# Kernel tuning notes

Hardware: AMD Instinct MI355X
Metric: run time of the kernel (lower is better)

Reference implementation:

```python
import jax, jax.numpy as jnp
import numpy as np

HIDDEN = 512
NUM_HEAD = 8
HEAD_DIM = HIDDEN // NUM_HEAD


def setup_inputs() -> dict:
    key = jax.random.key(0)
    ks = jax.random.split(key, 12)
    B, S = 8, 1024
    inp = {
        "v": jax.random.normal(ks[0], (B, S, HIDDEN), dtype=jnp.float32),
        "k": jax.random.normal(ks[1], (B, S, HIDDEN), dtype=jnp.float32),
        "q": jax.random.normal(ks[2], (B, S, HIDDEN), dtype=jnp.float32),
        "mask": jnp.zeros((B, 1, 1, S), dtype=bool),
    }
    scale = 1.0 / np.sqrt(HIDDEN)
    inp["Wv"] = jax.random.normal(ks[3], (HIDDEN, HIDDEN), dtype=jnp.float32) * scale
    inp["bv"] = jax.random.normal(ks[4], (HIDDEN,), dtype=jnp.float32) * scale
    inp["Wk"] = jax.random.normal(ks[5], (HIDDEN, HIDDEN), dtype=jnp.float32) * scale
    inp["bk"] = jax.random.normal(ks[6], (HIDDEN,), dtype=jnp.float32) * scale
    inp["Wq"] = jax.random.normal(ks[7], (HIDDEN, HIDDEN), dtype=jnp.float32) * scale
    inp["bq"] = jax.random.normal(ks[8], (HIDDEN,), dtype=jnp.float32) * scale
    inp["Wm"] = jax.random.normal(ks[9], (HIDDEN, HIDDEN), dtype=jnp.float32) * scale
    inp["bm"] = jax.random.normal(ks[10], (HIDDEN,), dtype=jnp.float32) * scale
    return inp


def _split_heads(x):
    # [B, S, H*D] -> [B, H, S, D]
    B, S, _ = x.shape
    return x.reshape(B, S, NUM_HEAD, HEAD_DIM).transpose(0, 2, 1, 3)


def reference(v, k, q, mask, Wv, bv, Wk, bk, Wq, bq, Wm, bm):
    B, S, _ = q.shape
    # linear projections (torch Linear: x @ W.T + b)
    vh = _split_heads(v @ Wv.T + bv)
    kh = _split_heads(k @ Wk.T + bk)
    qh = _split_heads(q @ Wq.T + bq)
    scale = 1.0 / jnp.sqrt(jnp.asarray(HEAD_DIM, dtype=qh.dtype))
    scores = jnp.einsum('bhqd,bhkd->bhqk', qh, kh) * scale
    scores = jnp.where(mask, jnp.asarray(-10000.0, dtype=scores.dtype), scores)
    att_map = jax.nn.softmax(scores, axis=-1)
    atted = jnp.einsum('bhqk,bhkd->bhqd', att_map, vh)
    atted = atted.transpose(0, 2, 1, 3).reshape(B, S, HIDDEN)
    atted = atted @ Wm.T + bm
    return atted, att_map
```

## Files before the change

### kernel.cpp

```cpp
#include <hip/hip_runtime.h>
#include <cstddef>

#define SEQ 1024
#define HID 512
#define NH 8
#define HD 64

typedef __attribute__((ext_vector_type(8))) short bf16x8;
typedef __attribute__((ext_vector_type(4))) float f32x4;

__device__ inline unsigned short f2bf(float f) {
  unsigned u = __builtin_bit_cast(unsigned, f);
  return (unsigned short)((u + 0x7fffu + ((u >> 16) & 1u)) >> 16);
}

template <int MODE>
__global__ __launch_bounds__(256) void proj_mfma(const void* __restrict__ Xv,
                                                 const float* __restrict__ W,
                                                 const float* __restrict__ bias,
                                                 void* __restrict__ outv) {
  __shared__ short As[128 * 64];
  __shared__ short Bs[128 * 64];

  const int t = threadIdx.x;
  const int lane = t & 63, wid = t >> 6;
  const int lg = lane >> 4, lr = lane & 15;
  const int wm = (wid >> 1) * 64, wn = (wid & 1) * 64;
  const int m0 = blockIdx.y * 128, n0 = blockIdx.x * 128;

  f32x4 acc[4][4];
  const f32x4 zf = {0.f, 0.f, 0.f, 0.f};
#pragma unroll
  for (int mg = 0; mg < 4; ++mg)
#pragma unroll
    for (int ng = 0; ng < 4; ++ng) acc[mg][ng] = zf;

  for (int k0 = 0; k0 < 512; k0 += 64) {
    __syncthreads();
#pragma unroll
    for (int i = 0; i < 4; ++i) {
      const int gi = t + i * 256;
      const int r = gi >> 3, g = gi & 7;
      const int dst = r * 64 + ((g ^ (r & 7)) * 8);
      if (MODE == 2) {
        const unsigned short* Xb = (const unsigned short*)Xv;
        *reinterpret_cast<bf16x8*>(As + dst) =
            *reinterpret_cast<const bf16x8*>(Xb + (size_t)(m0 + r) * 512 + k0 + g * 8);
      } else {
        const float* X = (const float*)Xv;
        const float* src = X + (size_t)(m0 + r) * 512 + k0 + g * 8;
        const float4 a = *reinterpret_cast<const float4*>(src);
        const float4 b2 = *reinterpret_cast<const float4*>(src + 4);
        union { bf16x8 v; unsigned short u[8]; } p;
        p.u[0] = f2bf(a.x);  p.u[1] = f2bf(a.y);  p.u[2] = f2bf(a.z);  p.u[3] = f2bf(a.w);
        p.u[4] = f2bf(b2.x); p.u[5] = f2bf(b2.y); p.u[6] = f2bf(b2.z); p.u[7] = f2bf(b2.w);
        *reinterpret_cast<bf16x8*>(As + dst) = p.v;
      }
      const float* srcw = W + (size_t)(n0 + r) * 512 + k0 + g * 8;
      const float4 wa = *reinterpret_cast<const float4*>(srcw);
      const float4 wb = *reinterpret_cast<const float4*>(srcw + 4);
      union { bf16x8 v; unsigned short u[8]; } q;
      q.u[0] = f2bf(wa.x); q.u[1] = f2bf(wa.y); q.u[2] = f2bf(wa.z); q.u[3] = f2bf(wa.w);
      q.u[4] = f2bf(wb.x); q.u[5] = f2bf(wb.y); q.u[6] = f2bf(wb.z); q.u[7] = f2bf(wb.w);
      *reinterpret_cast<bf16x8*>(Bs + dst) = q.v;
    }
    __syncthreads();

#pragma unroll
    for (int c = 0; c < 2; ++c) {
      bf16x8 af[4], bf[4];
#pragma unroll
      for (int mg = 0; mg < 4; ++mg) {
        const int r = wm + mg * 16 + lr;
        af[mg] = *reinterpret_cast<const bf16x8*>(As + r * 64 + (((lg + 4 * c) ^ (r & 7)) * 8));
      }
#pragma unroll
      for (int ng = 0; ng < 4; ++ng) {
        const int r = wn + ng * 16 + lr;
        bf[ng] = *reinterpret_cast<const bf16x8*>(Bs + r * 64 + (((lg + 4 * c) ^ (r & 7)) * 8));
      }
#pragma unroll
      for (int mg = 0; mg < 4; ++mg)
#pragma unroll
        for (int ng = 0; ng < 4; ++ng)
          acc[mg][ng] =
              __builtin_amdgcn_mfma_f32_16x16x32_bf16(af[mg], bf[ng], acc[mg][ng], 0, 0, 0);
    }
  }

  float bv[4];
#pragma unroll
  for (int ng = 0; ng < 4; ++ng) bv[ng] = bias[n0 + wn + ng * 16 + lr];

#pragma unroll
  for (int mg = 0; mg < 4; ++mg) {
#pragma unroll
    for (int reg = 0; reg < 4; ++reg) {
      const int m = m0 + wm + mg * 16 + 4 * lg + reg;
#pragma unroll
      for (int ng = 0; ng < 4; ++ng) {
        const int n = n0 + wn + ng * 16 + lr;
        float cval = acc[mg][ng][reg] + bv[ng];
        if (MODE == 2) {
          ((float*)outv)[(size_t)m * 512 + n] = cval;
        } else {
          if (MODE == 1) cval *= 0.125f;
          const int b = m >> 10, s = m & 1023, h = n >> 6, d = n & 63;
          ((unsigned short*)outv)[(((size_t)(b * NH + h)) * SEQ + s) * HD + d] = f2bf(cval);
        }
      }
    }
  }
}

__global__ __launch_bounds__(256) void attn_mfma(const unsigned short* __restrict__ qh,
                                                 const unsigned short* __restrict__ kh,
                                                 const unsigned short* __restrict__ vh,
                                                 const unsigned char* __restrict__ mask,
                                                 float* __restrict__ att_map,
                                                 unsigned short* __restrict__ atted) {
  __shared__ short Ks[128 * 64];
  __shared__ short Vt[64 * 128];
  __shared__ short Ps[4][2048];

  const int t = threadIdx.x;
  const int lane = t & 63, wid = t >> 6;
  const int lg = lane >> 4, lr = lane & 15;
  const int qt = blockIdx.x & 15;
  const int bh = blockIdx.x >> 4;
  const int b = bh >> 3, h = bh & 7;
  const int q0 = qt * 64 + wid * 16;

  const unsigned short* Qb = qh + ((size_t)bh * SEQ + q0) * HD;
  const unsigned short* Kb = kh + (size_t)bh * SEQ * HD;
  const unsigned short* Vb = vh + (size_t)bh * SEQ * HD;
  const unsigned char* mrow = mask + (size_t)b * SEQ;

  bf16x8 qf[2];
#pragma unroll
  for (int c = 0; c < 2; ++c)
    qf[c] = *reinterpret_cast<const bf16x8*>(Qb + (size_t)lr * HD + lg * 8 + 32 * c);

  float rs0 = 0.f, rs1 = 0.f, rs2 = 0.f, rs3 = 0.f;
  for (int kt = 0; kt < 8; ++kt) {
    __syncthreads();
#pragma unroll
    for (int i = 0; i < 4; ++i) {
      const int gi = t + i * 256;
      const int r = gi >> 3, g = gi & 7;
      *reinterpret_cast<bf16x8*>(Ks + r * 64 + ((g ^ (r & 7)) * 8)) =
          *reinterpret_cast<const bf16x8*>(Kb + (size_t)(kt * 128 + r) * HD + g * 8);
    }
    __syncthreads();
#pragma unroll
    for (int cg = 0; cg < 8; ++cg) {
      f32x4 s = {0.f, 0.f, 0.f, 0.f};
#pragma unroll
      for (int c = 0; c < 2; ++c) {
        const int r = cg * 16 + lr;
        const bf16x8 kf =
            *reinterpret_cast<const bf16x8*>(Ks + r * 64 + (((lg + 4 * c) ^ (r & 7)) * 8));
        s = __builtin_amdgcn_mfma_f32_16x16x32_bf16(qf[c], kf, s, 0, 0, 0);
      }
      const int kpos = kt * 128 + cg * 16 + lr;
      if (!mrow[kpos]) {
        rs0 += __expf(s[0]); rs1 += __expf(s[1]);
        rs2 += __expf(s[2]); rs3 += __expf(s[3]);
      }
    }
  }
#pragma unroll
  for (int m = 1; m <= 8; m <<= 1) {
    rs0 += __shfl_xor(rs0, m); rs1 += __shfl_xor(rs1, m);
    rs2 += __shfl_xor(rs2, m); rs3 += __shfl_xor(rs3, m);
  }
  const float inv0 = 1.f / rs0, inv1 = 1.f / rs1, inv2 = 1.f / rs2, inv3 = 1.f / rs3;

  const f32x4 zf = {0.f, 0.f, 0.f, 0.f};
  f32x4 oacc[4] = {zf, zf, zf, zf};
  short* Pw = Ps[wid];

  for (int kt = 0; kt < 8; ++kt) {
    __syncthreads();
#pragma unroll
    for (int i = 0; i < 4; ++i) {
      const int gi = t + i * 256;
      const int r = gi >> 3, g = gi & 7;
      *reinterpret_cast<bf16x8*>(Ks + r * 64 + ((g ^ (r & 7)) * 8)) =
          *reinterpret_cast<const bf16x8*>(Kb + (size_t)(kt * 128 + r) * HD + g * 8);
      union { bf16x8 v; unsigned short u[8]; } vv;
      vv.v = *reinterpret_cast<const bf16x8*>(Vb + (size_t)(kt * 128 + r) * HD + g * 8);
#pragma unroll
      for (int j = 0; j < 8; ++j) {
        const int d = g * 8 + j;
        Vt[d * 128 + (((r >> 3) ^ (d & 7)) * 8) + (r & 7)] = (short)vv.u[j];
      }
    }
    __syncthreads();

#pragma unroll
    for (int cg = 0; cg < 8; ++cg) {
      f32x4 s = {0.f, 0.f, 0.f, 0.f};
#pragma unroll
      for (int c = 0; c < 2; ++c) {
        const int r = cg * 16 + lr;
        const bf16x8 kf =
            *reinterpret_cast<const bf16x8*>(Ks + r * 64 + (((lg + 4 * c) ^ (r & 7)) * 8));
        s = __builtin_amdgcn_mfma_f32_16x16x32_bf16(qf[c], kf, s, 0, 0, 0);
      }
      const int kpos = kt * 128 + cg * 16 + lr;
      const bool msk = mrow[kpos];
      float p[4];
      p[0] = msk ? 0.f : __expf(s[0]) * inv0;
      p[1] = msk ? 0.f : __expf(s[1]) * inv1;
      p[2] = msk ? 0.f : __expf(s[2]) * inv2;
      p[3] = msk ? 0.f : __expf(s[3]) * inv3;
      const int col = cg * 16 + lr;
#pragma unroll
      for (int reg = 0; reg < 4; ++reg) {
        const int row = 4 * lg + reg;
        att_map[((size_t)bh * SEQ + (q0 + row)) * SEQ + kpos] = p[reg];
        Pw[row * 128 + (((col >> 3) ^ (row & 7)) * 8) + (col & 7)] = (short)f2bf(p[reg]);
      }
    }

    bf16x8 pa[4];
#pragma unroll
    for (int c = 0; c < 4; ++c)
      pa[c] = *reinterpret_cast<const bf16x8*>(Pw + lr * 128 + (((lg + 4 * c) ^ (lr & 7)) * 8));
#pragma unroll
    for (int ng = 0; ng < 4; ++ng) {
      const int d = ng * 16 + lr;
#pragma unroll
      for (int c = 0; c < 4; ++c) {
        const bf16x8 vf =
            *reinterpret_cast<const bf16x8*>(Vt + d * 128 + (((lg + 4 * c) ^ (d & 7)) * 8));
        oacc[ng] = __builtin_amdgcn_mfma_f32_16x16x32_bf16(pa[c], vf, oacc[ng], 0, 0, 0);
      }
    }
  }

#pragma unroll
  for (int ng = 0; ng < 4; ++ng) {
#pragma unroll
    for (int reg = 0; reg < 4; ++reg) {
      const int q = q0 + 4 * lg + reg;
      const int d = ng * 16 + lr;
      atted[((size_t)b * SEQ + q) * HID + h * HD + d] = f2bf(oacc[ng][reg]);
    }
  }
}

extern "C" void kernel_launch(void* const* d_in, const int* in_sizes, int n_in,
                              void* d_out, int out_size, void* d_ws, size_t ws_size,
                              hipStream_t stream) {
  const float* v = (const float*)d_in[0];
  const float* k = (const float*)d_in[1];
  const float* q = (const float*)d_in[2];
  const unsigned char* mask = (const unsigned char*)d_in[3];
  const float* Wv = (const float*)d_in[4];
  const float* bv = (const float*)d_in[5];
  const float* Wk = (const float*)d_in[6];
  const float* bk = (const float*)d_in[7];
  const float* Wq = (const float*)d_in[8];
  const float* bq = (const float*)d_in[9];
  const float* Wm = (const float*)d_in[10];
  const float* bm = (const float*)d_in[11];

  float* out_atted = (float*)d_out;
  float* out_att = out_atted + (size_t)8 * SEQ * HID;

  const size_t TN = (size_t)8 * SEQ * HID;
  unsigned short* qh = (unsigned short*)d_ws;
  unsigned short* kh = qh + TN;
  unsigned short* vh = kh + TN;
  unsigned short* aw = vh + TN;

  const dim3 gg(4, 64);
  proj_mfma<1><<<gg, 256, 0, stream>>>(q, Wq, bq, qh);
  proj_mfma<0><<<gg, 256, 0, stream>>>(k, Wk, bk, kh);
  proj_mfma<0><<<gg, 256, 0, stream>>>(v, Wv, bv, vh);

  attn_mfma<<<dim3(1024), 256, 0, stream>>>(qh, kh, vh, mask, out_att, aw);

  proj_mfma<2><<<gg, 256, 0, stream>>>(aw, Wm, bm, out_atted);
}
```

Measured before the change: 228.5 us.

## Single-pass attention with register-held probabilities and merged QKV projection launch

Removes the separate row-sum pass over K by accumulating exp scores and the unnormalized P·V in one sweep. Unnormalized bf16 probabilities are kept in registers, normalized once at the end, and written to att_map as vectorized nontemporal stores; the output rows are scaled by the inverse sum. The mask becomes an additive float table in shared memory, and the three QKV projections are merged into one launch via blockIdx.z. In exchange, att_map is now derived from bf16-rounded probabilities, which loses precision, and the 64-entry register array raises VGPR pressure.

```diff
diff --git a/kernel.cpp b/kernel.cpp
--- a/kernel.cpp
+++ b/kernel.cpp
@@ -13,14 +13,28 @@
   unsigned u = __builtin_bit_cast(unsigned, f);
   return (unsigned short)((u + 0x7fffu + ((u >> 16) & 1u)) >> 16);
 }
-
-template <int MODE>
-__global__ __launch_bounds__(256) void proj_mfma(const void* __restrict__ Xv,
-                                                 const float* __restrict__ W,
-                                                 const float* __restrict__ bias,
-                                                 void* __restrict__ outv) {
+__device__ inline float bfhi2f(unsigned u) {
+  return __builtin_bit_cast(float, u & 0xffff0000u);
+}
+__device__ inline float bflo2f(unsigned u) {
+  return __builtin_bit_cast(float, u << 16);
+}
+
+__global__ __launch_bounds__(256) void proj_qkv(
+    const float* __restrict__ x0, const float* __restrict__ x1, const float* __restrict__ x2,
+    const float* __restrict__ w0, const float* __restrict__ w1, const float* __restrict__ w2,
+    const float* __restrict__ b0, const float* __restrict__ b1, const float* __restrict__ b2,
+    unsigned short* __restrict__ o0, unsigned short* __restrict__ o1,
+    unsigned short* __restrict__ o2) {
   __shared__ short As[128 * 64];
   __shared__ short Bs[128 * 64];
+
+  const int z = blockIdx.z;
+  const float* X = z == 0 ? x0 : (z == 1 ? x1 : x2);
+  const float* W = z == 0 ? w0 : (z == 1 ? w1 : w2);
+  const float* bias = z == 0 ? b0 : (z == 1 ? b1 : b2);
+  unsigned short* out = z == 0 ? o0 : (z == 1 ? o1 : o2);
+  const float scale = z == 0 ? 0.125f : 1.0f;
 
   const int t = threadIdx.x;
   const int lane = t & 63, wid = t >> 6;
@@ -42,12 +56,7 @@
       const int gi = t + i * 256;
       const int r = gi >> 3, g = gi & 7;
       const int dst = r * 64 + ((g ^ (r & 7)) * 8);
-      if (MODE == 2) {
-        const unsigned short* Xb = (const unsigned short*)Xv;
-        *reinterpret_cast<bf16x8*>(As + dst) =
-            *reinterpret_cast<const bf16x8*>(Xb + (size_t)(m0 + r) * 512 + k0 + g * 8);
-      } else {
-        const float* X = (const float*)Xv;
+      {
         const float* src = X + (size_t)(m0 + r) * 512 + k0 + g * 8;
         const float4 a = *reinterpret_cast<const float4*>(src);
         const float4 b2 = *reinterpret_cast<const float4*>(src + 4);
@@ -56,6 +65,89 @@
         p.u[4] = f2bf(b2.x); p.u[5] = f2bf(b2.y); p.u[6] = f2bf(b2.z); p.u[7] = f2bf(b2.w);
         *reinterpret_cast<bf16x8*>(As + dst) = p.v;
       }
+      {
+        const float* srcw = W + (size_t)(n0 + r) * 512 + k0 + g * 8;
+        const float4 wa = *reinterpret_cast<const float4*>(srcw);
+        const float4 wb = *reinterpret_cast<const float4*>(srcw + 4);
+        union { bf16x8 v; unsigned short u[8]; } q;
+        q.u[0] = f2bf(wa.x); q.u[1] = f2bf(wa.y); q.u[2] = f2bf(wa.z); q.u[3] = f2bf(wa.w);
+        q.u[4] = f2bf(wb.x); q.u[5] = f2bf(wb.y); q.u[6] = f2bf(wb.z); q.u[7] = f2bf(wb.w);
+        *reinterpret_cast<bf16x8*>(Bs + dst) = q.v;
+      }
+    }
+    __syncthreads();
+
+#pragma unroll
+    for (int c = 0; c < 2; ++c) {
+      bf16x8 af[4], bfr[4];
+#pragma unroll
+      for (int mg = 0; mg < 4; ++mg) {
+        const int r = wm + mg * 16 + lr;
+        af[mg] = *reinterpret_cast<const bf16x8*>(As + r * 64 + (((lg + 4 * c) ^ (r & 7)) * 8));
+      }
+#pragma unroll
+      for (int ng = 0; ng < 4; ++ng) {
+        const int r = wn + ng * 16 + lr;
+        bfr[ng] = *reinterpret_cast<const bf16x8*>(Bs + r * 64 + (((lg + 4 * c) ^ (r & 7)) * 8));
+      }
+#pragma unroll
+      for (int mg = 0; mg < 4; ++mg)
+#pragma unroll
+        for (int ng = 0; ng < 4; ++ng)
+          acc[mg][ng] =
+              __builtin_amdgcn_mfma_f32_16x16x32_bf16(af[mg], bfr[ng], acc[mg][ng], 0, 0, 0);
+    }
+  }
+
+  float bv[4];
+#pragma unroll
+  for (int ng = 0; ng < 4; ++ng) bv[ng] = bias[n0 + wn + ng * 16 + lr];
+
+#pragma unroll
+  for (int mg = 0; mg < 4; ++mg) {
+#pragma unroll
+    for (int reg = 0; reg < 4; ++reg) {
+      const int m = m0 + wm + mg * 16 + 4 * lg + reg;
+#pragma unroll
+      for (int ng = 0; ng < 4; ++ng) {
+        const int n = n0 + wn + ng * 16 + lr;
+        const float cval = (acc[mg][ng][reg] + bv[ng]) * scale;
+        const int b = m >> 10, s = m & 1023, h = n >> 6, d = n & 63;
+        out[(((size_t)(b * NH + h)) * SEQ + s) * HD + d] = f2bf(cval);
+      }
+    }
+  }
+}
+
+__global__ __launch_bounds__(256) void proj_out(const unsigned short* __restrict__ Xb,
+                                                const float* __restrict__ W,
+                                                const float* __restrict__ bias,
+                                                float* __restrict__ outv) {
+  __shared__ short As[128 * 64];
+  __shared__ short Bs[128 * 64];
+
+  const int t = threadIdx.x;
+  const int lane = t & 63, wid = t >> 6;
+  const int lg = lane >> 4, lr = lane & 15;
+  const int wm = (wid >> 1) * 64, wn = (wid & 1) * 64;
+  const int m0 = blockIdx.y * 128, n0 = blockIdx.x * 128;
+
+  f32x4 acc[4][4];
+  const f32x4 zf = {0.f, 0.f, 0.f, 0.f};
+#pragma unroll
+  for (int mg = 0; mg < 4; ++mg)
+#pragma unroll
+    for (int ng = 0; ng < 4; ++ng) acc[mg][ng] = zf;
+
+  for (int k0 = 0; k0 < 512; k0 += 64) {
+    __syncthreads();
+#pragma unroll
+    for (int i = 0; i < 4; ++i) {
+      const int gi = t + i * 256;
+      const int r = gi >> 3, g = gi & 7;
+      const int dst = r * 64 + ((g ^ (r & 7)) * 8);
+      *reinterpret_cast<bf16x8*>(As + dst) =
+          *reinterpret_cast<const bf16x8*>(Xb + (size_t)(m0 + r) * 512 + k0 + g * 8);
       const float* srcw = W + (size_t)(n0 + r) * 512 + k0 + g * 8;
       const float4 wa = *reinterpret_cast<const float4*>(srcw);
       const float4 wb = *reinterpret_cast<const float4*>(srcw + 4);
@@ -68,7 +160,7 @@
 
 #pragma unroll
     for (int c = 0; c < 2; ++c) {
-      bf16x8 af[4], bf[4];
+      bf16x8 af[4], bfr[4];
 #pragma unroll
       for (int mg = 0; mg < 4; ++mg) {
         const int r = wm + mg * 16 + lr;
@@ -77,14 +169,14 @@
 #pragma unroll
       for (int ng = 0; ng < 4; ++ng) {
         const int r = wn + ng * 16 + lr;
-        bf[ng] = *reinterpret_cast<const bf16x8*>(Bs + r * 64 + (((lg + 4 * c) ^ (r & 7)) * 8));
+        bfr[ng] = *reinterpret_cast<const bf16x8*>(Bs + r * 64 + (((lg + 4 * c) ^ (r & 7)) * 8));
       }
 #pragma unroll
       for (int mg = 0; mg < 4; ++mg)
 #pragma unroll
         for (int ng = 0; ng < 4; ++ng)
           acc[mg][ng] =
-              __builtin_amdgcn_mfma_f32_16x16x32_bf16(af[mg], bf[ng], acc[mg][ng], 0, 0, 0);
+              __builtin_amdgcn_mfma_f32_16x16x32_bf16(af[mg], bfr[ng], acc[mg][ng], 0, 0, 0);
     }
   }
 
@@ -100,14 +192,7 @@
 #pragma unroll
       for (int ng = 0; ng < 4; ++ng) {
         const int n = n0 + wn + ng * 16 + lr;
-        float cval = acc[mg][ng][reg] + bv[ng];
-        if (MODE == 2) {
-          ((float*)outv)[(size_t)m * 512 + n] = cval;
-        } else {
-          if (MODE == 1) cval *= 0.125f;
-          const int b = m >> 10, s = m & 1023, h = n >> 6, d = n & 63;
-          ((unsigned short*)outv)[(((size_t)(b * NH + h)) * SEQ + s) * HD + d] = f2bf(cval);
-        }
+        __builtin_nontemporal_store(acc[mg][ng][reg] + bv[ng], outv + (size_t)m * 512 + n);
       }
     }
   }
@@ -121,7 +206,8 @@
                                                  unsigned short* __restrict__ atted) {
   __shared__ short Ks[128 * 64];
   __shared__ short Vt[64 * 128];
-  __shared__ short Ps[4][2048];
+  __shared__ short Pw4[4][2048];
+  __shared__ float maskf[1024];
 
   const int t = threadIdx.x;
   const int lane = t & 63, wid = t >> 6;
@@ -136,50 +222,24 @@
   const unsigned short* Vb = vh + (size_t)bh * SEQ * HD;
   const unsigned char* mrow = mask + (size_t)b * SEQ;
 
+#pragma unroll
+  for (int i = 0; i < 4; ++i) {
+    const int idx = t + i * 256;
+    maskf[idx] = mrow[idx] ? -10000.f : 0.f;
+  }
+
   bf16x8 qf[2];
 #pragma unroll
   for (int c = 0; c < 2; ++c)
     qf[c] = *reinterpret_cast<const bf16x8*>(Qb + (size_t)lr * HD + lg * 8 + 32 * c);
 
-  float rs0 = 0.f, rs1 = 0.f, rs2 = 0.f, rs3 = 0.f;
-  for (int kt = 0; kt < 8; ++kt) {
-    __syncthreads();
-#pragma unroll
-    for (int i = 0; i < 4; ++i) {
-      const int gi = t + i * 256;
-      const int r = gi >> 3, g = gi & 7;
-      *reinterpret_cast<bf16x8*>(Ks + r * 64 + ((g ^ (r & 7)) * 8)) =
-          *reinterpret_cast<const bf16x8*>(Kb + (size_t)(kt * 128 + r) * HD + g * 8);
-    }
-    __syncthreads();
-#pragma unroll
-    for (int cg = 0; cg < 8; ++cg) {
-      f32x4 s = {0.f, 0.f, 0.f, 0.f};
-#pragma unroll
-      for (int c = 0; c < 2; ++c) {
-        const int r = cg * 16 + lr;
-        const bf16x8 kf =
-            *reinterpret_cast<const bf16x8*>(Ks + r * 64 + (((lg + 4 * c) ^ (r & 7)) * 8));
-        s = __builtin_amdgcn_mfma_f32_16x16x32_bf16(qf[c], kf, s, 0, 0, 0);
-      }
-      const int kpos = kt * 128 + cg * 16 + lr;
-      if (!mrow[kpos]) {
-        rs0 += __expf(s[0]); rs1 += __expf(s[1]);
-        rs2 += __expf(s[2]); rs3 += __expf(s[3]);
-      }
-    }
-  }
-#pragma unroll
-  for (int m = 1; m <= 8; m <<= 1) {
-    rs0 += __shfl_xor(rs0, m); rs1 += __shfl_xor(rs1, m);
-    rs2 += __shfl_xor(rs2, m); rs3 += __shfl_xor(rs3, m);
-  }
-  const float inv0 = 1.f / rs0, inv1 = 1.f / rs1, inv2 = 1.f / rs2, inv3 = 1.f / rs3;
-
+  uint2 pk[64];
+  float rs = 0.f;
   const f32x4 zf = {0.f, 0.f, 0.f, 0.f};
   f32x4 oacc[4] = {zf, zf, zf, zf};
-  short* Pw = Ps[wid];
-
+  short* Pw = Pw4[wid];
+
+#pragma unroll
   for (int kt = 0; kt < 8; ++kt) {
     __syncthreads();
 #pragma unroll
@@ -200,53 +260,69 @@
 
 #pragma unroll
     for (int cg = 0; cg < 8; ++cg) {
-      f32x4 s = {0.f, 0.f, 0.f, 0.f};
+      f32x4 s = zf;
 #pragma unroll
       for (int c = 0; c < 2; ++c) {
         const int r = cg * 16 + lr;
         const bf16x8 kf =
             *reinterpret_cast<const bf16x8*>(Ks + r * 64 + (((lg + 4 * c) ^ (r & 7)) * 8));
-        s = __builtin_amdgcn_mfma_f32_16x16x32_bf16(qf[c], kf, s, 0, 0, 0);
-      }
-      const int kpos = kt * 128 + cg * 16 + lr;
-      const bool msk = mrow[kpos];
-      float p[4];
-      p[0] = msk ? 0.f : __expf(s[0]) * inv0;
-      p[1] = msk ? 0.f : __expf(s[1]) * inv1;
-      p[2] = msk ? 0.f : __expf(s[2]) * inv2;
-      p[3] = msk ? 0.f : __expf(s[3]) * inv3;
-      const int col = cg * 16 + lr;
-#pragma unroll
-      for (int reg = 0; reg < 4; ++reg) {
-        const int row = 4 * lg + reg;
-        att_map[((size_t)bh * SEQ + (q0 + row)) * SEQ + kpos] = p[reg];
-        Pw[row * 128 + (((col >> 3) ^ (row & 7)) * 8) + (col & 7)] = (short)f2bf(p[reg]);
-      }
-    }
-
-    bf16x8 pa[4];
-#pragma unroll
-    for (int c = 0; c < 4; ++c)
-      pa[c] = *reinterpret_cast<const bf16x8*>(Pw + lr * 128 + (((lg + 4 * c) ^ (lr & 7)) * 8));
-#pragma unroll
-    for (int ng = 0; ng < 4; ++ng) {
-      const int d = ng * 16 + lr;
-#pragma unroll
-      for (int c = 0; c < 4; ++c) {
+        s = __builtin_amdgcn_mfma_f32_16x16x32_bf16(kf, qf[c], s, 0, 0, 0);
+      }
+      const float4 madd =
+          *reinterpret_cast<const float4*>(maskf + kt * 128 + cg * 16 + 4 * lg);
+      const float p0 = __expf(s[0] + madd.x);
+      const float p1 = __expf(s[1] + madd.y);
+      const float p2 = __expf(s[2] + madd.z);
+      const float p3 = __expf(s[3] + madd.w);
+      rs += (p0 + p1) + (p2 + p3);
+      uint2 pr;
+      pr.x = (unsigned)f2bf(p0) | ((unsigned)f2bf(p1) << 16);
+      pr.y = (unsigned)f2bf(p2) | ((unsigned)f2bf(p3) << 16);
+      pk[kt * 8 + cg] = pr;
+      const int gk = 2 * cg + (lg >> 1);
+      *reinterpret_cast<uint2*>(Pw + lr * 128 + ((gk ^ (lr & 7)) * 8) + (lg & 1) * 4) = pr;
+    }
+
+#pragma unroll
+    for (int c = 0; c < 4; ++c) {
+      const bf16x8 pa =
+          *reinterpret_cast<const bf16x8*>(Pw + lr * 128 + (((lg + 4 * c) ^ (lr & 7)) * 8));
+#pragma unroll
+      for (int ng = 0; ng < 4; ++ng) {
+        const int d = ng * 16 + lr;
         const bf16x8 vf =
             *reinterpret_cast<const bf16x8*>(Vt + d * 128 + (((lg + 4 * c) ^ (d & 7)) * 8));
-        oacc[ng] = __builtin_amdgcn_mfma_f32_16x16x32_bf16(pa[c], vf, oacc[ng], 0, 0, 0);
-      }
-    }
-  }
-
+        oacc[ng] = __builtin_amdgcn_mfma_f32_16x16x32_bf16(pa, vf, oacc[ng], 0, 0, 0);
+      }
+    }
+  }
+
+  rs += __shfl_xor(rs, 16);
+  rs += __shfl_xor(rs, 32);
+  const float inv = 1.f / rs;
+
+  float* arow = att_map + ((size_t)bh * SEQ + q0 + lr) * SEQ + 4 * lg;
+#pragma unroll
+  for (int cg = 0; cg < 64; ++cg) {
+    const uint2 pr = pk[cg];
+    f32x4 w;
+    w.x = bflo2f(pr.x) * inv;
+    w.y = bfhi2f(pr.x) * inv;
+    w.z = bflo2f(pr.y) * inv;
+    w.w = bfhi2f(pr.y) * inv;
+    __builtin_nontemporal_store(w, reinterpret_cast<f32x4*>(arow + cg * 16));
+  }
+
+  float invq[4];
+#pragma unroll
+  for (int reg = 0; reg < 4; ++reg) invq[reg] = __shfl(inv, 4 * lg + reg);
 #pragma unroll
   for (int ng = 0; ng < 4; ++ng) {
 #pragma unroll
     for (int reg = 0; reg < 4; ++reg) {
       const int q = q0 + 4 * lg + reg;
       const int d = ng * 16 + lr;
-      atted[((size_t)b * SEQ + q) * HID + h * HD + d] = f2bf(oacc[ng][reg]);
+      atted[((size_t)b * SEQ + q) * HID + h * HD + d] = f2bf(oacc[ng][reg] * invq[reg]);
     }
   }
 }
@@ -276,12 +352,9 @@
   unsigned short* vh = kh + TN;
   unsigned short* aw = vh + TN;
 
-  const dim3 gg(4, 64);
-  proj_mfma<1><<<gg, 256, 0, stream>>>(q, Wq, bq, qh);
-  proj_mfma<0><<<gg, 256, 0, stream>>>(k, Wk, bk, kh);
-  proj_mfma<0><<<gg, 256, 0, stream>>>(v, Wv, bv, vh);
+  proj_qkv<<<dim3(4, 64, 3), 256, 0, stream>>>(q, k, v, Wq, Wk, Wv, bq, bk, bv, qh, kh, vh);
 
   attn_mfma<<<dim3(1024), 256, 0, stream>>>(qh, kh, vh, mask, out_att, aw);
 
-  proj_mfma<2><<<gg, 256, 0, stream>>>(aw, Wm, bm, out_atted);
-}
+  proj_out<<<dim3(4, 64), 256, 0, stream>>>(aw, Wm, bm, out_atted);
+}
```

After: 266.3 us. 1.17x slower.
